# Optimization experiments

Measured on AMD Instinct MI355X. Metric: run time of the kernel, lower is better.

Reference implementation:

```python
import jax, jax.numpy as jnp
import numpy as np

NSITES = 64   # 2 * nphysical spin-orbital sites
BOND = 128    # MPS bond dimension D
BATCH = 16384 # sampled occupation configurations


def setup_inputs() -> dict:
    key = jax.random.key(0)
    k1, k2, k3, k4 = jax.random.split(key, 4)
    # Site tensors A[k, n] in R^{D x D}; scaled so chain products stay O(1).
    data = jax.random.normal(k1, (NSITES, 2, BOND, BOND), dtype=jnp.float32) / jnp.sqrt(jnp.float32(BOND))
    left = jax.random.normal(k2, (BOND,), dtype=jnp.float32)
    right = jax.random.normal(k3, (BOND,), dtype=jnp.float32)
    # Occupation-number vectors (0/1 per spin orbital).
    onstate = jax.random.randint(k4, (BATCH, NSITES), 0, 2, dtype=jnp.int32)
    # Orbital-ordering permutation (identity here).
    image2 = jnp.arange(NSITES, dtype=jnp.int32)
    return {"onstate": onstate, "data": data, "left": left, "right": right, "image2": image2}


def reference(onstate, data, left, right, image2):
    # Reorder physical indices per the stored orbital image: [B, NSITES]
    occ = onstate[:, image2]
    B = occ.shape[0]
    D = left.shape[0]
    v0 = jnp.broadcast_to(left, (B, D))  # left boundary, batched

    def step(v, xs):
        A, n = xs  # A: [2, D, D] site tensor, n: [B] occupations at this site
        # Contract with both quantum-number blocks, then select per sample
        # (equivalent to gathering the block indexed by the occupation).
        v_new = jnp.where((n == 1)[:, None], v @ A[1], v @ A[0])  # [B, D]
        return v_new, None

    vT, _ = jax.lax.scan(step, v0, (data, occ.T))
    return vT @ right  # amplitudes psi(n): [B]
```

## Files before the change

### kernel.cpp

```cpp
#include <hip/hip_runtime.h>
#include <hip/hip_bf16.h>

#define NS 64
#define NP 32
#define DIM 128
#define BATCH_N 16384

typedef float f32x4 __attribute__((ext_vector_type(4)));
typedef _Float16 f16x8 __attribute__((ext_vector_type(8)));
typedef unsigned int u32;
typedef unsigned long long u64;

__device__ __forceinline__ unsigned short f2h(float f) {
    _Float16 h = (_Float16)f;
    return __builtin_bit_cast(unsigned short, h);
}

__global__ __launch_bounds__(256)
void prep_pair_frags(const float* __restrict__ data,
                     unsigned short* __restrict__ afrag) {
    __shared__ float LA[2 * 32 * 129];
    __shared__ float LB[2 * 32 * 128];

    const int p   = blockIdx.x >> 2;
    const int kk  = blockIdx.x & 3;
    const int tid = threadIdx.x;
    const int kgrp = tid >> 5;
    const int mgrp = tid & 31;

    const float* A0 = data + ((size_t)(2 * p) * 2 + 0) * DIM * DIM;
    const float* A1 = A0 + DIM * DIM;
    const float* B0 = data + ((size_t)(2 * p + 1) * 2 + 0) * DIM * DIM;
    const float* B1 = B0 + DIM * DIM;

    for (int c = tid; c < 32 * DIM; c += 256) {
        int kl = c >> 7, j = c & 127;
        float a0 = A0[(kk * 32 + kl) * DIM + j];
        float a1 = A1[(kk * 32 + kl) * DIM + j];
        LA[kl * 129 + j] = a0;
        LA[32 * 129 + kl * 129 + j] = a1 - a0;
    }

    float acc[2][2][4][4];
#pragma unroll
    for (int L = 0; L < 2; ++L)
#pragma unroll
        for (int R = 0; R < 2; ++R)
#pragma unroll
            for (int i = 0; i < 4; ++i)
#pragma unroll
                for (int mi = 0; mi < 4; ++mi) acc[L][R][i][mi] = 0.f;

    for (int ch = 0; ch < 4; ++ch) {
        __syncthreads();
        for (int c = tid; c < 32 * DIM; c += 256) {
            int jl = c >> 7, m = c & 127;
            float b0 = B0[(ch * 32 + jl) * DIM + m];
            float b1 = B1[(ch * 32 + jl) * DIM + m];
            LB[jl * 128 + m] = b0;
            LB[4096 + jl * 128 + m] = b1 - b0;
        }
        __syncthreads();
#pragma unroll 2
        for (int jl = 0; jl < 32; ++jl) {
            int j = ch * 32 + jl;
            float la0[4], la1[4];
#pragma unroll
            for (int i = 0; i < 4; ++i) {
                la0[i] = LA[(kgrp * 4 + i) * 129 + j];
                la1[i] = LA[32 * 129 + (kgrp * 4 + i) * 129 + j];
            }
            f32x4 lb0 = *reinterpret_cast<const f32x4*>(&LB[jl * 128 + mgrp * 4]);
            f32x4 lb1 = *reinterpret_cast<const f32x4*>(&LB[4096 + jl * 128 + mgrp * 4]);
#pragma unroll
            for (int i = 0; i < 4; ++i)
#pragma unroll
                for (int mi = 0; mi < 4; ++mi) {
                    acc[0][0][i][mi] += la0[i] * lb0[mi];
                    acc[1][0][i][mi] += la1[i] * lb0[mi];
                    acc[0][1][i][mi] += la0[i] * lb1[mi];
                    acc[1][1][i][mi] += la1[i] * lb1[mi];
                }
        }
    }

#pragma unroll
    for (int t = 0; t < 4; ++t) {
        int L = t & 1, R = t >> 1;
#pragma unroll
        for (int i = 0; i < 4; ++i)
#pragma unroll
            for (int mi = 0; mi < 4; ++mi) {
                int k = kk * 32 + kgrp * 4 + i;
                int m = mgrp * 4 + mi;
                int g = (k & 31) >> 3, j = k & 7;
                int lane = g * 16 + (m & 15);
                int mm = m >> 4;
                size_t idx =
                    ((((((size_t)p * 4 + t) * 4 + kk) * 8 + mm) * 64 + lane) * 8) + j;
                afrag[idx] = f2h(acc[L][R][i][mi]);
            }
    }
}

__global__ void prep_bits(const int* __restrict__ onstate,
                          const int* __restrict__ image2,
                          u64* __restrict__ bits) {
    int r = blockIdx.x * blockDim.x + threadIdx.x;
    if (r >= BATCH_N) return;
    const int* row = onstate + (size_t)r * NS;
    u64 b = 0;
#pragma unroll 8
    for (int t = 0; t < NS; ++t) {
        b |= ((u64)(row[image2[t]] & 1)) << t;
    }
    bits[r] = b;
}

__global__ __launch_bounds__(512, 4)
void mps_pair(const unsigned short* __restrict__ afrag,
              const u64* __restrict__ occbits,
              const float* __restrict__ left,
              const float* __restrict__ right,
              float* __restrict__ out) {
    __shared__ unsigned short vlds[2][32 * DIM];
    __shared__ float red[32][33];

    const int tid  = threadIdx.x;
    const int wid  = tid >> 6;
    const int lane = tid & 63;
    const int li   = lane & 15;
    const int g    = lane >> 4;
    const int rbase = blockIdx.x * 32;

    u64 bits[2];
#pragma unroll
    for (int rg = 0; rg < 2; ++rg)
        bits[rg] = occbits[rbase + rg * 16 + li];

    u32 rdoff[2][4];
#pragma unroll
    for (int rg = 0; rg < 2; ++rg)
#pragma unroll
        for (int kk = 0; kk < 4; ++kk) {
            int r = rg * 16 + li;
            rdoff[rg][kk] =
                (u32)(r * 256 + kk * 64 + g * 16) ^ ((u32)(r & 7) << 4);
        }
    u32 wroff[2];
#pragma unroll
    for (int rg = 0; rg < 2; ++rg) {
        int r = rg * 16 + li;
        int mbase = wid * 16 + g * 4;
        wroff[rg] = (u32)(r * 256 + mbase * 2) ^ ((u32)(r & 7) << 4);
    }

    if (tid < 32 * 16) {
        int r  = tid >> 4;
        int kc = tid & 15;
        unsigned short tmp[8];
#pragma unroll
        for (int j = 0; j < 8; ++j) tmp[j] = f2h(left[kc * 8 + j]);
        u32 byte = (u32)(r * 256 + kc * 16) ^ ((u32)(r & 7) << 4);
        *reinterpret_cast<uint4*>(reinterpret_cast<char*>(&vlds[0][0]) + byte) =
            *reinterpret_cast<uint4*>(tmp);
    }
    __syncthreads();

    const f16x8 zf = {0, 0, 0, 0, 0, 0, 0, 0};

    f16x8 ft0[4][2], ft1[4][2];
    f32x4 acc[2];

#define ISSUE_CHUNK(FT, P_, H_)                                               \
    {                                                                         \
        const unsigned short* sb_ = afrag + (size_t)(P_) * 65536;             \
        _Pragma("unroll")                                                     \
        for (int t = 0; t < 4; ++t)                                           \
            _Pragma("unroll")                                                 \
            for (int kq = 0; kq < 2; ++kq)                                    \
                FT[t][kq] = *reinterpret_cast<const f16x8*>(                  \
                    sb_ +                                                     \
                    ((size_t)((t * 4 + 2 * (H_) + kq) * 8 + wid) * 512) +     \
                    lane * 8);                                                \
    }

#define COMPUTE_HALF(P_, H_, FT)                                              \
    {                                                                         \
        const int p_ = (P_);                                                  \
        const char* vb = reinterpret_cast<const char*>(&vlds[p_ & 1][0]);     \
        _Pragma("unroll")                                                     \
        for (int kq = 0; kq < 2; ++kq) {                                      \
            const int kk = 2 * (H_) + kq;                                     \
            f16x8 bfr[2];                                                     \
            _Pragma("unroll")                                                 \
            for (int rg = 0; rg < 2; ++rg)                                    \
                bfr[rg] =                                                     \
                    *reinterpret_cast<const f16x8*>(vb + rdoff[rg][kk]);      \
            _Pragma("unroll")                                                 \
            for (int rg = 0; rg < 2; ++rg) {                                  \
                bool m0 = (bits[rg] >> (2 * p_)) & 1;                         \
                bool m1 = (bits[rg] >> (2 * p_ + 1)) & 1;                     \
                f16x8 vb0  = m0 ? bfr[rg] : zf;                               \
                f16x8 vb1  = m1 ? bfr[rg] : zf;                               \
                f16x8 vb01 = m1 ? vb0 : zf;                                   \
                acc[rg] = __builtin_amdgcn_mfma_f32_16x16x32_f16(             \
                    FT[0][kq], bfr[rg], acc[rg], 0, 0, 0);                    \
                acc[rg] = __builtin_amdgcn_mfma_f32_16x16x32_f16(             \
                    FT[1][kq], vb0, acc[rg], 0, 0, 0);                        \
                acc[rg] = __builtin_amdgcn_mfma_f32_16x16x32_f16(             \
                    FT[2][kq], vb1, acc[rg], 0, 0, 0);                        \
                acc[rg] = __builtin_amdgcn_mfma_f32_16x16x32_f16(             \
                    FT[3][kq], vb01, acc[rg], 0, 0, 0);                       \
            }                                                                 \
        }                                                                     \
    }

#define WRITE_PHASE(P_)                                                       \
    {                                                                         \
        const int p_ = (P_);                                                  \
        char* wb = reinterpret_cast<char*>(&vlds[(p_ + 1) & 1][0]);           \
        if (p_ < NP - 1) {                                                    \
            _Pragma("unroll")                                                 \
            for (int rg = 0; rg < 2; ++rg) {                                  \
                u32 lo = ((u32)f2h(acc[rg][1]) << 16) | f2h(acc[rg][0]);      \
                u32 hi = ((u32)f2h(acc[rg][3]) << 16) | f2h(acc[rg][2]);      \
                uint2 w = {lo, hi};                                           \
                *reinterpret_cast<uint2*>(wb + wroff[rg]) = w;                \
            }                                                                 \
            __syncthreads();                                                  \
        } else {                                                              \
            int mcol = wid * 16 + g * 4;                                      \
            const float4 rv = *reinterpret_cast<const float4*>(right + mcol); \
            _Pragma("unroll")                                                 \
            for (int rg = 0; rg < 2; ++rg) {                                  \
                float pv = acc[rg][0] * rv.x + acc[rg][1] * rv.y +            \
                           acc[rg][2] * rv.z + acc[rg][3] * rv.w;             \
                red[rg * 16 + li][wid * 4 + g] = pv;                          \
            }                                                                 \
            __syncthreads();                                                  \
            if (tid < 32) {                                                   \
                float ssum = 0.f;                                             \
                _Pragma("unroll")                                             \
                for (int i = 0; i < 32; ++i) ssum += red[tid][i];             \
                out[rbase + tid] = ssum;                                      \
            }                                                                 \
        }                                                                     \
    }

    ISSUE_CHUNK(ft0, 0, 0);
    for (int p = 0; p < NP; ++p) {
        acc[0] = (f32x4){0.f, 0.f, 0.f, 0.f};
        acc[1] = (f32x4){0.f, 0.f, 0.f, 0.f};
        ISSUE_CHUNK(ft1, p, 1);
        COMPUTE_HALF(p, 0, ft0);
        if (p + 1 < NP) ISSUE_CHUNK(ft0, p + 1, 0);
        COMPUTE_HALF(p, 1, ft1);
        WRITE_PHASE(p);
    }

#undef ISSUE_CHUNK
#undef COMPUTE_HALF
#undef WRITE_PHASE
}

extern "C" void kernel_launch(void* const* d_in, const int* in_sizes, int n_in,
                              void* d_out, int out_size, void* d_ws, size_t ws_size,
                              hipStream_t stream) {
    const int*   onstate = (const int*)d_in[0];
    const float* data    = (const float*)d_in[1];
    const float* left    = (const float*)d_in[2];
    const float* right   = (const float*)d_in[3];
    const int*   image2  = (const int*)d_in[4];
    float* out = (float*)d_out;

    unsigned short* afrag = (unsigned short*)d_ws;
    u64* bits = (u64*)((char*)d_ws + (size_t)2097152 * sizeof(unsigned short));

    prep_pair_frags<<<128, 256, 0, stream>>>(data, afrag);
    prep_bits<<<64, 256, 0, stream>>>(onstate, image2, bits);
    mps_pair<<<512, 512, 0, stream>>>(afrag, bits, left, right, out);
}
```

Measured before the change: 126.9 us.

## Reorder pair fragments per wave, split prep grid, add setprio and packed converts

The prep kernel now splits each block's output columns in half, doubling the grid to 256 blocks with smaller per-thread tiles. It also writes fragments in a layout where each wave's per-half chunk is contiguous, so the main kernel can load them with simple precomputed offsets. The main kernel raises wave priority around the MFMA sections and uses packed round-toward-zero fp16 conversion for the state write-back. Rounding mode changes from nearest to toward zero, which slightly alters numerics.

```diff
diff --git a/kernel.cpp b/kernel.cpp
--- a/kernel.cpp
+++ b/kernel.cpp
@@ -8,6 +8,7 @@
 
 typedef float f32x4 __attribute__((ext_vector_type(4)));
 typedef _Float16 f16x8 __attribute__((ext_vector_type(8)));
+typedef __fp16 fp16x2 __attribute__((ext_vector_type(2)));
 typedef unsigned int u32;
 typedef unsigned long long u64;
 
@@ -20,13 +21,14 @@
 void prep_pair_frags(const float* __restrict__ data,
                      unsigned short* __restrict__ afrag) {
     __shared__ float LA[2 * 32 * 129];
-    __shared__ float LB[2 * 32 * 128];
-
-    const int p   = blockIdx.x >> 2;
-    const int kk  = blockIdx.x & 3;
+    __shared__ float LB[2 * 32 * 68];
+
+    const int p   = blockIdx.x >> 3;
+    const int kk  = (blockIdx.x >> 1) & 3;
+    const int mh  = blockIdx.x & 1;
     const int tid = threadIdx.x;
-    const int kgrp = tid >> 5;
-    const int mgrp = tid & 31;
+    const int kgrp = tid >> 4;
+    const int mgrp = tid & 15;
 
     const float* A0 = data + ((size_t)(2 * p) * 2 + 0) * DIM * DIM;
     const float* A1 = A0 + DIM * DIM;
@@ -41,39 +43,39 @@
         LA[32 * 129 + kl * 129 + j] = a1 - a0;
     }
 
-    float acc[2][2][4][4];
+    float acc[2][2][2][4];
 #pragma unroll
     for (int L = 0; L < 2; ++L)
 #pragma unroll
         for (int R = 0; R < 2; ++R)
 #pragma unroll
-            for (int i = 0; i < 4; ++i)
+            for (int i = 0; i < 2; ++i)
 #pragma unroll
                 for (int mi = 0; mi < 4; ++mi) acc[L][R][i][mi] = 0.f;
 
     for (int ch = 0; ch < 4; ++ch) {
         __syncthreads();
-        for (int c = tid; c < 32 * DIM; c += 256) {
-            int jl = c >> 7, m = c & 127;
-            float b0 = B0[(ch * 32 + jl) * DIM + m];
-            float b1 = B1[(ch * 32 + jl) * DIM + m];
-            LB[jl * 128 + m] = b0;
-            LB[4096 + jl * 128 + m] = b1 - b0;
+        for (int c = tid; c < 32 * 64; c += 256) {
+            int jl = c >> 6, ml = c & 63;
+            float b0 = B0[(ch * 32 + jl) * DIM + mh * 64 + ml];
+            float b1 = B1[(ch * 32 + jl) * DIM + mh * 64 + ml];
+            LB[jl * 68 + ml] = b0;
+            LB[32 * 68 + jl * 68 + ml] = b1 - b0;
         }
         __syncthreads();
 #pragma unroll 2
         for (int jl = 0; jl < 32; ++jl) {
             int j = ch * 32 + jl;
-            float la0[4], la1[4];
-#pragma unroll
-            for (int i = 0; i < 4; ++i) {
-                la0[i] = LA[(kgrp * 4 + i) * 129 + j];
-                la1[i] = LA[32 * 129 + (kgrp * 4 + i) * 129 + j];
+            float la0[2], la1[2];
+#pragma unroll
+            for (int i = 0; i < 2; ++i) {
+                la0[i] = LA[(kgrp * 2 + i) * 129 + j];
+                la1[i] = LA[32 * 129 + (kgrp * 2 + i) * 129 + j];
             }
-            f32x4 lb0 = *reinterpret_cast<const f32x4*>(&LB[jl * 128 + mgrp * 4]);
-            f32x4 lb1 = *reinterpret_cast<const f32x4*>(&LB[4096 + jl * 128 + mgrp * 4]);
-#pragma unroll
-            for (int i = 0; i < 4; ++i)
+            f32x4 lb0 = *reinterpret_cast<const f32x4*>(&LB[jl * 68 + mgrp * 4]);
+            f32x4 lb1 = *reinterpret_cast<const f32x4*>(&LB[32 * 68 + jl * 68 + mgrp * 4]);
+#pragma unroll
+            for (int i = 0; i < 2; ++i)
 #pragma unroll
                 for (int mi = 0; mi < 4; ++mi) {
                     acc[0][0][i][mi] += la0[i] * lb0[mi];
@@ -84,20 +86,23 @@
         }
     }
 
+    const int H   = kk >> 1;
+    const int kq  = kk & 1;
 #pragma unroll
     for (int t = 0; t < 4; ++t) {
         int L = t & 1, R = t >> 1;
 #pragma unroll
-        for (int i = 0; i < 4; ++i)
+        for (int i = 0; i < 2; ++i)
 #pragma unroll
             for (int mi = 0; mi < 4; ++mi) {
-                int k = kk * 32 + kgrp * 4 + i;
-                int m = mgrp * 4 + mi;
-                int g = (k & 31) >> 3, j = k & 7;
-                int lane = g * 16 + (m & 15);
+                int k = kk * 32 + kgrp * 2 + i;
+                int m = mh * 64 + mgrp * 4 + mi;
                 int mm = m >> 4;
+                int lane = ((k & 31) >> 3) * 16 + (m & 15);
+                int jj = k & 7;
                 size_t idx =
-                    ((((((size_t)p * 4 + t) * 4 + kk) * 8 + mm) * 64 + lane) * 8) + j;
+                    ((size_t)((((p * 8 + mm) * 2 + H) * 4 + t) * 2 + kq)) * 512 +
+                    lane * 8 + jj;
                 afrag[idx] = f2h(acc[L][R][i][mi]);
             }
     }
@@ -138,6 +143,9 @@
     for (int rg = 0; rg < 2; ++rg)
         bits[rg] = occbits[rbase + rg * 16 + li];
 
+    const int voff0 = wid * 8192 + 2048 + lane * 8;
+    const int voff1 = voff0 + 4096;
+
     u32 rdoff[2][4];
 #pragma unroll
     for (int rg = 0; rg < 2; ++rg)
@@ -172,23 +180,21 @@
     f16x8 ft0[4][2], ft1[4][2];
     f32x4 acc[2];
 
-#define ISSUE_CHUNK(FT, P_, H_)                                               \
+#define ISSUE_CHUNK(FT, PB, VOFF)                                             \
     {                                                                         \
-        const unsigned short* sb_ = afrag + (size_t)(P_) * 65536;             \
         _Pragma("unroll")                                                     \
         for (int t = 0; t < 4; ++t)                                           \
             _Pragma("unroll")                                                 \
             for (int kq = 0; kq < 2; ++kq)                                    \
                 FT[t][kq] = *reinterpret_cast<const f16x8*>(                  \
-                    sb_ +                                                     \
-                    ((size_t)((t * 4 + 2 * (H_) + kq) * 8 + wid) * 512) +     \
-                    lane * 8);                                                \
+                    (PB) + (VOFF) + (t * 1024 + kq * 512 - 2048));            \
     }
 
 #define COMPUTE_HALF(P_, H_, FT)                                              \
     {                                                                         \
         const int p_ = (P_);                                                  \
         const char* vb = reinterpret_cast<const char*>(&vlds[p_ & 1][0]);     \
+        __builtin_amdgcn_s_setprio(1);                                        \
         _Pragma("unroll")                                                     \
         for (int kq = 0; kq < 2; ++kq) {                                      \
             const int kk = 2 * (H_) + kq;                                     \
@@ -214,6 +220,7 @@
                     FT[3][kq], vb01, acc[rg], 0, 0, 0);                       \
             }                                                                 \
         }                                                                     \
+        __builtin_amdgcn_s_setprio(0);                                        \
     }
 
 #define WRITE_PHASE(P_)                                                       \
@@ -223,9 +230,10 @@
         if (p_ < NP - 1) {                                                    \
             _Pragma("unroll")                                                 \
             for (int rg = 0; rg < 2; ++rg) {                                  \
-                u32 lo = ((u32)f2h(acc[rg][1]) << 16) | f2h(acc[rg][0]);      \
-                u32 hi = ((u32)f2h(acc[rg][3]) << 16) | f2h(acc[rg][2]);      \
-                uint2 w = {lo, hi};                                           \
+                fp16x2 h01 = __builtin_amdgcn_cvt_pkrtz(acc[rg][0], acc[rg][1]); \
+                fp16x2 h23 = __builtin_amdgcn_cvt_pkrtz(acc[rg][2], acc[rg][3]); \
+                uint2 w = {__builtin_bit_cast(u32, h01),                      \
+                           __builtin_bit_cast(u32, h23)};                     \
                 *reinterpret_cast<uint2*>(wb + wroff[rg]) = w;                \
             }                                                                 \
             __syncthreads();                                                  \
@@ -248,13 +256,17 @@
         }                                                                     \
     }
 
-    ISSUE_CHUNK(ft0, 0, 0);
+    ISSUE_CHUNK(ft0, afrag, voff0);
     for (int p = 0; p < NP; ++p) {
+        const unsigned short* pb = afrag + ((size_t)p << 16);
         acc[0] = (f32x4){0.f, 0.f, 0.f, 0.f};
         acc[1] = (f32x4){0.f, 0.f, 0.f, 0.f};
-        ISSUE_CHUNK(ft1, p, 1);
+        ISSUE_CHUNK(ft1, pb, voff1);
         COMPUTE_HALF(p, 0, ft0);
-        if (p + 1 < NP) ISSUE_CHUNK(ft0, p + 1, 0);
+        if (p + 1 < NP) {
+            const unsigned short* pbn = pb + 65536;
+            ISSUE_CHUNK(ft0, pbn, voff0);
+        }
         COMPUTE_HALF(p, 1, ft1);
         WRITE_PHASE(p);
     }
@@ -277,7 +289,7 @@
     unsigned short* afrag = (unsigned short*)d_ws;
     u64* bits = (u64*)((char*)d_ws + (size_t)2097152 * sizeof(unsigned short));
 
-    prep_pair_frags<<<128, 256, 0, stream>>>(data, afrag);
+    prep_pair_frags<<<256, 256, 0, stream>>>(data, afrag);
     prep_bits<<<64, 256, 0, stream>>>(onstate, image2, bits);
     mps_pair<<<512, 512, 0, stream>>>(afrag, bits, left, right, out);
 }
```

Result: faster. 118.7 us (-6.4%).
